# Kernel optimization log

Measured on AMD Instinct MI355X. Metric: run time of the kernel, lower is better.

The kernel has to match this reference:

```python
import jax, jax.numpy as jnp
import numpy as np

B, V, H_DIM, W_DIM = 4, 4, 256, 384
D_SH = 1  # sh_degree=0, pred_color=False -> (0+1)^2
SCALE_MIN, SCALE_MAX = 1e-05, 30.0
EPS = 1e-08


def _quat_to_mat(q):  # (...,4) wxyz unit quat -> (...,3,3)
    w, x, y, z = q[..., 0], q[..., 1], q[..., 2], q[..., 3]
    return jnp.stack([
        jnp.stack([1 - 2 * (y * y + z * z), 2 * (x * y - w * z), 2 * (x * z + w * y)], -1),
        jnp.stack([2 * (x * y + w * z), 1 - 2 * (x * x + z * z), 2 * (y * z - w * x)], -1),
        jnp.stack([2 * (x * z - w * y), 2 * (y * z + w * x), 1 - 2 * (x * x + y * y)], -1),
    ], -2)


def _mat_to_quat_wxyz(m):  # (...,3,3) rotation -> (...,4) wxyz
    m00, m01, m02 = m[..., 0, 0], m[..., 0, 1], m[..., 0, 2]
    m10, m11, m12 = m[..., 1, 0], m[..., 1, 1], m[..., 1, 2]
    m20, m21, m22 = m[..., 2, 0], m[..., 2, 1], m[..., 2, 2]
    q_abs = jnp.sqrt(jnp.maximum(0.0, jnp.stack([
        1.0 + m00 + m11 + m22, 1.0 + m00 - m11 - m22,
        1.0 - m00 + m11 - m22, 1.0 - m00 - m11 + m22], -1)))
    cand = jnp.stack([
        jnp.stack([q_abs[..., 0] ** 2, m21 - m12, m02 - m20, m10 - m01], -1),
        jnp.stack([m21 - m12, q_abs[..., 1] ** 2, m10 + m01, m02 + m20], -1),
        jnp.stack([m02 - m20, m10 + m01, q_abs[..., 2] ** 2, m12 + m21], -1),
        jnp.stack([m10 - m01, m20 + m02, m21 + m12, q_abs[..., 3] ** 2], -1),
    ], -2)
    cand = cand / (2.0 * jnp.maximum(q_abs[..., None], 0.1))
    idx = jnp.argmax(q_abs, axis=-1)
    q = jnp.take_along_axis(cand, idx[..., None, None], axis=-2)[..., 0, :]
    return q / jnp.linalg.norm(q, axis=-1, keepdims=True)


def _quat_mul_wxyz(a, b):
    aw, ax, ay, az = a[..., 0], a[..., 1], a[..., 2], a[..., 3]
    bw, bx, by, bz = b[..., 0], b[..., 1], b[..., 2], b[..., 3]
    return jnp.stack([
        aw * bw - ax * bx - ay * by - az * bz,
        aw * bx + ax * bw + ay * bz - az * by,
        aw * by - ax * bz + ay * bw + az * bx,
        aw * bz + ax * by - ay * bx + az * bw], -1)


def setup_inputs() -> dict:
    key = jax.random.key(0)
    k1, k2, k3, k4, k5, k6 = jax.random.split(key, 6)
    # valid world->cam extrinsics: rotation from random unit quats + translation
    q = jax.random.normal(k1, (B, V, 4), jnp.float32)
    q = q / jnp.linalg.norm(q, axis=-1, keepdims=True)
    R = _quat_to_mat(q)
    t = jax.random.normal(k2, (B, V, 3), jnp.float32)
    ext = jnp.zeros((B, V, 4, 4), jnp.float32)
    ext = ext.at[..., :3, :3].set(R).at[..., :3, 3].set(t).at[..., 3, 3].set(1.0)
    # pixel-unit intrinsics
    f = W_DIM * (0.8 + 0.4 * jax.random.uniform(k3, (B, V), jnp.float32))
    intr = jnp.zeros((B, V, 3, 3), jnp.float32)
    intr = (intr.at[..., 0, 0].set(f).at[..., 1, 1].set(f)
                .at[..., 0, 2].set(W_DIM / 2).at[..., 1, 2].set(H_DIM / 2)
                .at[..., 2, 2].set(1.0))
    depths = 0.5 + 9.5 * jax.random.uniform(k4, (B, V, H_DIM, W_DIM), jnp.float32)
    opac = jax.random.uniform(k5, (B, V, H_DIM, W_DIM), jnp.float32)
    raw = jax.random.normal(k6, (B, V, H_DIM, W_DIM, 12), jnp.float32)
    return {"extrinsics": ext, "intrinsics": intr, "depths": depths,
            "opacities": opac, "raw_gaussians": raw, "H": H_DIM, "W": W_DIM}


def reference(extrinsics, intrinsics, depths, opacities, raw_gaussians, H, W):
    raw = raw_gaussians
    b, v = raw.shape[:2]
    dtype = raw.dtype
    # cam2world = affine inverse of world2cam extrinsics
    Rw2c = extrinsics[..., :3, :3]
    t = extrinsics[..., :3, 3]
    Rc2w = jnp.swapaxes(Rw2c, -1, -2)                       # (b,v,3,3)
    origins = -jnp.einsum('bvij,bvj->bvi', Rc2w, t)          # (b,v,3) camera centers
    # normalized intrinsics (detached in the original)
    intr_n = jax.lax.stop_gradient(intrinsics) * jnp.array(
        [[1.0 / W], [1.0 / H], [1.0]], dtype=intrinsics.dtype)
    # pixel-center grid in normalized [0,1] coords, (x, y) order
    xs = (jnp.arange(W, dtype=dtype) + 0.5) / W
    ys = (jnp.arange(H, dtype=dtype) + 0.5) / H
    xy = jnp.stack(jnp.meshgrid(xs, ys, indexing='xy'), -1)  # (H,W,2)
    pixel_size = jnp.array([1.0 / W, 1.0 / H], dtype=dtype)
    xy = xy[None, None] + raw[..., :2] * pixel_size          # (b,v,H,W,2) with xy offset
    # unproject: K^-1 @ [x,y,1], normalize, rotate into world
    Kinv = jnp.linalg.inv(intr_n)                            # (b,v,3,3)
    homog = jnp.concatenate([xy, jnp.ones_like(xy[..., :1])], -1)
    d_cam = jnp.einsum('bvij,bvhwj->bvhwi', Kinv, homog)
    d_cam = d_cam / jnp.linalg.norm(d_cam, axis=-1, keepdims=True)
    d_world = jnp.einsum('bvij,bvhwj->bvhwi', Rc2w, d_cam)
    means = origins[:, :, None, None] + d_world * depths[..., None]
    means = means.reshape(b, -1, 3)
    # scales: sigmoid squash then metric scaling by depth * intrinsics multiplier
    scales = SCALE_MIN + (SCALE_MAX - SCALE_MIN) * jax.nn.sigmoid(raw[..., 2:5])
    k2 = intr_n[..., :2, :2]
    det = k2[..., 0, 0] * k2[..., 1, 1] - k2[..., 0, 1] * k2[..., 1, 0]
    inv2 = jnp.stack([
        jnp.stack([k2[..., 1, 1], -k2[..., 0, 1]], -1),
        jnp.stack([-k2[..., 1, 0], k2[..., 0, 0]], -1)], -2) / det[..., None, None]
    mult = 0.1 * jnp.einsum('bvij,j->bvi', inv2, pixel_size).sum(-1)  # (b,v)
    gs_scales = (scales * depths[..., None] * mult[:, :, None, None, None]).reshape(b, -1, 3)
    # rotations: normalize predicted cam quat (xyzw), compose with c2w rotation -> world wxyz
    rot = raw[..., 5:9]
    rot = rot / (jnp.linalg.norm(rot, axis=-1, keepdims=True) + EPS)
    cam_q_wxyz = jnp.concatenate([rot[..., 3:4], rot[..., :3]], -1)
    c2w_q = _mat_to_quat_wxyz(Rc2w)                          # (b,v,4)
    world_q = _quat_mul_wxyz(c2w_q[:, :, None, None, :], cam_q_wxyz)
    rotations = world_q.reshape(b, -1, 4)
    # spherical harmonics: degree 0 -> sh_mask is all ones, no SH rotation
    harmonics = raw[..., 9:12].reshape(b, -1, 3, D_SH)
    opac = opacities.reshape(b, -1)
    return means, gs_scales, rotations, harmonics, opac
```

## Files before the change

### kernel.cpp

```cpp
#include <hip/hip_runtime.h>
#include <math.h>

#define Bc 4
#define Vc 4
#define Hc 256
#define Wc 384
#define HWc (Hc*Wc)
#define TOTc (Bc*Vc*HWc)
#define SCALE_MIN_c 1e-05f
#define SCALE_MAX_c 30.0f
#define EPS_c 1e-08f

#define MEANS_OFF  ((size_t)0)
#define SCALES_OFF ((size_t)TOTc*3)
#define ROT_OFF    ((size_t)TOTc*6)
#define HARM_OFF   ((size_t)TOTc*10)
#define OPAC_OFF   ((size_t)TOTc*13)

__global__ __launch_bounds__(256) void ga_kernel(
    const float* __restrict__ ext,
    const float* __restrict__ intr,
    const float* __restrict__ depths,
    const float* __restrict__ opac,
    const float* __restrict__ raw,
    float* __restrict__ out)
{
    __shared__ float sR[9];
    __shared__ float sO[3];
    __shared__ float sK[9];
    __shared__ float sQ[4];
    __shared__ float sMult;

    const int tid = threadIdx.x;
    const int g   = blockIdx.x * 256 + tid;

    if (tid == 0) {
        const int view = blockIdx.x / (HWc / 256);
        const float* E = ext + view * 16;
        float R[9];
        #pragma unroll
        for (int i = 0; i < 3; i++)
            #pragma unroll
            for (int j = 0; j < 3; j++)
                R[i*3+j] = E[j*4+i];
        const float t0 = E[3], t1 = E[7], t2 = E[11];
        sO[0] = -(R[0]*t0 + R[1]*t1 + R[2]*t2);
        sO[1] = -(R[3]*t0 + R[4]*t1 + R[5]*t2);
        sO[2] = -(R[6]*t0 + R[7]*t1 + R[8]*t2);
        #pragma unroll
        for (int k = 0; k < 9; k++) sR[k] = R[k];

        const float* I = intr + view * 9;
        const float a00 = I[0]*(1.0f/Wc), a01 = I[1]*(1.0f/Wc), a02 = I[2]*(1.0f/Wc);
        const float a10 = I[3]*(1.0f/Hc), a11 = I[4]*(1.0f/Hc), a12 = I[5]*(1.0f/Hc);
        const float a20 = I[6],           a21 = I[7],           a22 = I[8];
        const float det = a00*(a11*a22 - a12*a21)
                        - a01*(a10*a22 - a12*a20)
                        + a02*(a10*a21 - a11*a20);
        const float id = 1.0f / det;
        sK[0] = (a11*a22 - a12*a21)*id;
        sK[1] = (a02*a21 - a01*a22)*id;
        sK[2] = (a01*a12 - a02*a11)*id;
        sK[3] = (a12*a20 - a10*a22)*id;
        sK[4] = (a00*a22 - a02*a20)*id;
        sK[5] = (a02*a10 - a00*a12)*id;
        sK[6] = (a10*a21 - a11*a20)*id;
        sK[7] = (a01*a20 - a00*a21)*id;
        sK[8] = (a00*a11 - a01*a10)*id;

        const float det2 = a00*a11 - a01*a10;
        const float psx = 1.0f/Wc, psy = 1.0f/Hc;
        sMult = 0.1f * ((a11*psx - a01*psy) + (-a10*psx + a00*psy)) / det2;

        const float m00 = R[0], m01 = R[1], m02 = R[2];
        const float m10 = R[3], m11 = R[4], m12 = R[5];
        const float m20 = R[6], m21 = R[7], m22 = R[8];
        float qa[4];
        qa[0] = sqrtf(fmaxf(0.0f, 1.0f + m00 + m11 + m22));
        qa[1] = sqrtf(fmaxf(0.0f, 1.0f + m00 - m11 - m22));
        qa[2] = sqrtf(fmaxf(0.0f, 1.0f - m00 + m11 - m22));
        qa[3] = sqrtf(fmaxf(0.0f, 1.0f - m00 - m11 + m22));
        float cand[4][4] = {
            { qa[0]*qa[0], m21 - m12,   m02 - m20,   m10 - m01 },
            { m21 - m12,   qa[1]*qa[1], m10 + m01,   m02 + m20 },
            { m02 - m20,   m10 + m01,   qa[2]*qa[2], m12 + m21 },
            { m10 - m01,   m20 + m02,   m21 + m12,   qa[3]*qa[3] } };
        int idx = 0;
        if (qa[1] > qa[idx]) idx = 1;
        if (qa[2] > qa[idx]) idx = 2;
        if (qa[3] > qa[idx]) idx = 3;
        const float dd = 1.0f / (2.0f * fmaxf(qa[idx], 0.1f));
        float q0 = cand[idx][0]*dd, q1 = cand[idx][1]*dd,
              q2 = cand[idx][2]*dd, q3 = cand[idx][3]*dd;
        const float qn = 1.0f / sqrtf(q0*q0 + q1*q1 + q2*q2 + q3*q3);
        sQ[0] = q0*qn; sQ[1] = q1*qn; sQ[2] = q2*qn; sQ[3] = q3*qn;
    }
    __syncthreads();

    const float4* rp = reinterpret_cast<const float4*>(raw + (size_t)g * 12);
    const float4 r0 = rp[0];
    const float4 r1 = rp[1];
    const float4 r2 = rp[2];

    const int pix = g % HWc;
    const int h = pix / Wc;
    const int w = pix % Wc;

    const float x = (w + 0.5f) * (1.0f/Wc) + r0.x * (1.0f/Wc);
    const float y = (h + 0.5f) * (1.0f/Hc) + r0.y * (1.0f/Hc);

    float dc0 = sK[0]*x + sK[1]*y + sK[2];
    float dc1 = sK[3]*x + sK[4]*y + sK[5];
    float dc2 = sK[6]*x + sK[7]*y + sK[8];
    const float inl = rsqrtf(dc0*dc0 + dc1*dc1 + dc2*dc2);
    dc0 *= inl; dc1 *= inl; dc2 *= inl;

    const float dw0 = sR[0]*dc0 + sR[1]*dc1 + sR[2]*dc2;
    const float dw1 = sR[3]*dc0 + sR[4]*dc1 + sR[5]*dc2;
    const float dw2 = sR[6]*dc0 + sR[7]*dc1 + sR[8]*dc2;

    const float dep = depths[g];

    out[MEANS_OFF + (size_t)g*3 + 0] = sO[0] + dw0 * dep;
    out[MEANS_OFF + (size_t)g*3 + 1] = sO[1] + dw1 * dep;
    out[MEANS_OFF + (size_t)g*3 + 2] = sO[2] + dw2 * dep;

    const float sm = dep * sMult;
    const float s0 = (SCALE_MIN_c + (SCALE_MAX_c - SCALE_MIN_c) / (1.0f + __expf(-r0.z))) * sm;
    const float s1 = (SCALE_MIN_c + (SCALE_MAX_c - SCALE_MIN_c) / (1.0f + __expf(-r0.w))) * sm;
    const float s2 = (SCALE_MIN_c + (SCALE_MAX_c - SCALE_MIN_c) / (1.0f + __expf(-r1.x))) * sm;
    out[SCALES_OFF + (size_t)g*3 + 0] = s0;
    out[SCALES_OFF + (size_t)g*3 + 1] = s1;
    out[SCALES_OFF + (size_t)g*3 + 2] = s2;

    const float rx = r1.y, ry = r1.z, rz = r1.w, rw = r2.x;
    const float rn = 1.0f / (sqrtf(rx*rx + ry*ry + rz*rz + rw*rw) + EPS_c);
    const float bw = rw*rn, bx = rx*rn, by = ry*rn, bz = rz*rn;
    const float aw = sQ[0], ax = sQ[1], ay = sQ[2], az = sQ[3];
    float4 wq;
    wq.x = aw*bw - ax*bx - ay*by - az*bz;
    wq.y = aw*bx + ax*bw + ay*bz - az*by;
    wq.z = aw*by - ax*bz + ay*bw + az*bx;
    wq.w = aw*bz + ax*by - ay*bx + az*bw;
    reinterpret_cast<float4*>(out + ROT_OFF)[g] = wq;

    out[HARM_OFF + (size_t)g*3 + 0] = r2.y;
    out[HARM_OFF + (size_t)g*3 + 1] = r2.z;
    out[HARM_OFF + (size_t)g*3 + 2] = r2.w;

    out[OPAC_OFF + g] = opac[g];
}

extern "C" void kernel_launch(void* const* d_in, const int* in_sizes, int n_in,
                              void* d_out, int out_size, void* d_ws, size_t ws_size,
                              hipStream_t stream) {
    const float* ext    = (const float*)d_in[0];
    const float* intr   = (const float*)d_in[1];
    const float* depths = (const float*)d_in[2];
    const float* opac   = (const float*)d_in[3];
    const float* raw    = (const float*)d_in[4];
    float* out = (float*)d_out;

    ga_kernel<<<TOTc / 256, 256, 0, stream>>>(ext, intr, depths, opac, raw, out);
}
```

Before: 170.4 us.

## Stage stride-3 outputs through shared memory for coalesced float4 stores

The means, scales and harmonics outputs, which were written as scalar stride-3 stores, are now gathered in a shared-memory tile and written back as contiguous float4 stores per block. The global loads of raw, depth and opacity are moved ahead of the thread-0 camera setup and the first barrier, so they can overlap with it. This adds 9 KB of LDS per block and a second barrier, which may lower occupancy.

```diff
diff --git a/kernel.cpp b/kernel.cpp
--- a/kernel.cpp
+++ b/kernel.cpp
@@ -30,9 +30,17 @@
     __shared__ float sK[9];
     __shared__ float sQ[4];
     __shared__ float sMult;
+    __shared__ float sOut[2304];
 
     const int tid = threadIdx.x;
     const int g   = blockIdx.x * 256 + tid;
+
+    const float4* rp = reinterpret_cast<const float4*>(raw + (size_t)g * 12);
+    const float4 r0 = rp[0];
+    const float4 r1 = rp[1];
+    const float4 r2 = rp[2];
+    const float dep = depths[g];
+    const float op  = opac[g];
 
     if (tid == 0) {
         const int view = blockIdx.x / (HWc / 256);
@@ -97,11 +105,6 @@
     }
     __syncthreads();
 
-    const float4* rp = reinterpret_cast<const float4*>(raw + (size_t)g * 12);
-    const float4 r0 = rp[0];
-    const float4 r1 = rp[1];
-    const float4 r2 = rp[2];
-
     const int pix = g % HWc;
     const int h = pix / Wc;
     const int w = pix % Wc;
@@ -119,19 +122,14 @@
     const float dw1 = sR[3]*dc0 + sR[4]*dc1 + sR[5]*dc2;
     const float dw2 = sR[6]*dc0 + sR[7]*dc1 + sR[8]*dc2;
 
-    const float dep = depths[g];
-
-    out[MEANS_OFF + (size_t)g*3 + 0] = sO[0] + dw0 * dep;
-    out[MEANS_OFF + (size_t)g*3 + 1] = sO[1] + dw1 * dep;
-    out[MEANS_OFF + (size_t)g*3 + 2] = sO[2] + dw2 * dep;
+    sOut[tid*3 + 0] = sO[0] + dw0 * dep;
+    sOut[tid*3 + 1] = sO[1] + dw1 * dep;
+    sOut[tid*3 + 2] = sO[2] + dw2 * dep;
 
     const float sm = dep * sMult;
-    const float s0 = (SCALE_MIN_c + (SCALE_MAX_c - SCALE_MIN_c) / (1.0f + __expf(-r0.z))) * sm;
-    const float s1 = (SCALE_MIN_c + (SCALE_MAX_c - SCALE_MIN_c) / (1.0f + __expf(-r0.w))) * sm;
-    const float s2 = (SCALE_MIN_c + (SCALE_MAX_c - SCALE_MIN_c) / (1.0f + __expf(-r1.x))) * sm;
-    out[SCALES_OFF + (size_t)g*3 + 0] = s0;
-    out[SCALES_OFF + (size_t)g*3 + 1] = s1;
-    out[SCALES_OFF + (size_t)g*3 + 2] = s2;
+    sOut[768 + tid*3 + 0] = (SCALE_MIN_c + (SCALE_MAX_c - SCALE_MIN_c) / (1.0f + __expf(-r0.z))) * sm;
+    sOut[768 + tid*3 + 1] = (SCALE_MIN_c + (SCALE_MAX_c - SCALE_MIN_c) / (1.0f + __expf(-r0.w))) * sm;
+    sOut[768 + tid*3 + 2] = (SCALE_MIN_c + (SCALE_MAX_c - SCALE_MIN_c) / (1.0f + __expf(-r1.x))) * sm;
 
     const float rx = r1.y, ry = r1.z, rz = r1.w, rw = r2.x;
     const float rn = 1.0f / (sqrtf(rx*rx + ry*ry + rz*rz + rw*rw) + EPS_c);
@@ -144,11 +142,23 @@
     wq.w = aw*bz + ax*by - ay*bx + az*bw;
     reinterpret_cast<float4*>(out + ROT_OFF)[g] = wq;
 
-    out[HARM_OFF + (size_t)g*3 + 0] = r2.y;
-    out[HARM_OFF + (size_t)g*3 + 1] = r2.z;
-    out[HARM_OFF + (size_t)g*3 + 2] = r2.w;
+    sOut[1536 + tid*3 + 0] = r2.y;
+    sOut[1536 + tid*3 + 1] = r2.z;
+    sOut[1536 + tid*3 + 2] = r2.w;
 
-    out[OPAC_OFF + g] = opac[g];
+    out[OPAC_OFF + g] = op;
+
+    __syncthreads();
+
+    const float4* sv = reinterpret_cast<const float4*>(sOut);
+    #pragma unroll
+    for (int i = tid; i < 576; i += 256) {
+        const int sec = i / 192;
+        const int j   = i - sec * 192;
+        const size_t base = (sec == 0 ? MEANS_OFF : (sec == 1 ? SCALES_OFF : HARM_OFF))
+                          + (size_t)blockIdx.x * 768;
+        reinterpret_cast<float4*>(out + base)[j] = sv[i];
+    }
 }
 
 extern "C" void kernel_launch(void* const* d_in, const int* in_sizes, int n_in,
```

Result: no change. 170.6 us (+0.1%).

## Process four pixels per thread with vectorized stores and per-thread view setup

Applied to the files above, without the earlier changes.

Each thread now handles four consecutive pixels, loading raw/depth/opacity as 16-byte vectors and packing means, scales, harmonics and opacities into float4 nontemporal stores instead of scalar 3-strided stores. The per-view camera setup is computed redundantly by every thread in registers, removing the shared memory and __syncthreads barrier. The grid shrinks by four, which raises register pressure and per-thread setup cost in exchange for wider, fully coalesced memory transactions.

```diff
diff --git a/kernel.cpp b/kernel.cpp
--- a/kernel.cpp
+++ b/kernel.cpp
@@ -1,5 +1,7 @@
 #include <hip/hip_runtime.h>
 #include <math.h>
+
+typedef float f4 __attribute__((ext_vector_type(4)));
 
 #define Bc 4
 #define Vc 4
@@ -17,6 +19,8 @@
 #define HARM_OFF   ((size_t)TOTc*10)
 #define OPAC_OFF   ((size_t)TOTc*13)
 
+#define BLOCKS_PER_VIEW (HWc/1024)
+
 __global__ __launch_bounds__(256) void ga_kernel(
     const float* __restrict__ ext,
     const float* __restrict__ intr,
@@ -25,130 +29,142 @@
     const float* __restrict__ raw,
     float* __restrict__ out)
 {
-    __shared__ float sR[9];
-    __shared__ float sO[3];
-    __shared__ float sK[9];
-    __shared__ float sQ[4];
-    __shared__ float sMult;
+    const int tid  = threadIdx.x;
+    const int bid  = blockIdx.x;
+    const int view = bid / BLOCKS_PER_VIEW;
+    const int pix0 = (bid - view * BLOCKS_PER_VIEW) * 1024 + tid * 4;
+    const size_t g0 = (size_t)view * HWc + (size_t)pix0;
 
-    const int tid = threadIdx.x;
-    const int g   = blockIdx.x * 256 + tid;
+    const f4* rp = reinterpret_cast<const f4*>(raw + g0 * 12);
+    f4 rw[12];
+    #pragma unroll
+    for (int i = 0; i < 12; i++) rw[i] = rp[i];
+    const f4 dep4 = *reinterpret_cast<const f4*>(depths + g0);
+    const f4 op4  = *reinterpret_cast<const f4*>(opac + g0);
 
-    if (tid == 0) {
-        const int view = blockIdx.x / (HWc / 256);
-        const float* E = ext + view * 16;
-        float R[9];
-        #pragma unroll
-        for (int i = 0; i < 3; i++)
-            #pragma unroll
-            for (int j = 0; j < 3; j++)
-                R[i*3+j] = E[j*4+i];
-        const float t0 = E[3], t1 = E[7], t2 = E[11];
-        sO[0] = -(R[0]*t0 + R[1]*t1 + R[2]*t2);
-        sO[1] = -(R[3]*t0 + R[4]*t1 + R[5]*t2);
-        sO[2] = -(R[6]*t0 + R[7]*t1 + R[8]*t2);
-        #pragma unroll
-        for (int k = 0; k < 9; k++) sR[k] = R[k];
+    const float* E = ext + view * 16;
+    const float R0 = E[0], R1 = E[4], R2 = E[8];
+    const float R3 = E[1], R4 = E[5], R5 = E[9];
+    const float R6 = E[2], R7 = E[6], R8 = E[10];
+    const float t0 = E[3], t1 = E[7], t2 = E[11];
+    const float O0 = -(R0*t0 + R1*t1 + R2*t2);
+    const float O1 = -(R3*t0 + R4*t1 + R5*t2);
+    const float O2 = -(R6*t0 + R7*t1 + R8*t2);
 
-        const float* I = intr + view * 9;
-        const float a00 = I[0]*(1.0f/Wc), a01 = I[1]*(1.0f/Wc), a02 = I[2]*(1.0f/Wc);
-        const float a10 = I[3]*(1.0f/Hc), a11 = I[4]*(1.0f/Hc), a12 = I[5]*(1.0f/Hc);
-        const float a20 = I[6],           a21 = I[7],           a22 = I[8];
-        const float det = a00*(a11*a22 - a12*a21)
-                        - a01*(a10*a22 - a12*a20)
-                        + a02*(a10*a21 - a11*a20);
-        const float id = 1.0f / det;
-        sK[0] = (a11*a22 - a12*a21)*id;
-        sK[1] = (a02*a21 - a01*a22)*id;
-        sK[2] = (a01*a12 - a02*a11)*id;
-        sK[3] = (a12*a20 - a10*a22)*id;
-        sK[4] = (a00*a22 - a02*a20)*id;
-        sK[5] = (a02*a10 - a00*a12)*id;
-        sK[6] = (a10*a21 - a11*a20)*id;
-        sK[7] = (a01*a20 - a00*a21)*id;
-        sK[8] = (a00*a11 - a01*a10)*id;
+    const float* I = intr + view * 9;
+    const float a00 = I[0]*(1.0f/Wc), a01 = I[1]*(1.0f/Wc), a02 = I[2]*(1.0f/Wc);
+    const float a10 = I[3]*(1.0f/Hc), a11 = I[4]*(1.0f/Hc), a12 = I[5]*(1.0f/Hc);
+    const float a20 = I[6],           a21 = I[7],           a22 = I[8];
+    const float det = a00*(a11*a22 - a12*a21)
+                    - a01*(a10*a22 - a12*a20)
+                    + a02*(a10*a21 - a11*a20);
+    const float id = 1.0f / det;
+    const float K0 = (a11*a22 - a12*a21)*id;
+    const float K1 = (a02*a21 - a01*a22)*id;
+    const float K2 = (a01*a12 - a02*a11)*id;
+    const float K3 = (a12*a20 - a10*a22)*id;
+    const float K4 = (a00*a22 - a02*a20)*id;
+    const float K5 = (a02*a10 - a00*a12)*id;
+    const float K6 = (a10*a21 - a11*a20)*id;
+    const float K7 = (a01*a20 - a00*a21)*id;
+    const float K8 = (a00*a11 - a01*a10)*id;
 
-        const float det2 = a00*a11 - a01*a10;
-        const float psx = 1.0f/Wc, psy = 1.0f/Hc;
-        sMult = 0.1f * ((a11*psx - a01*psy) + (-a10*psx + a00*psy)) / det2;
+    const float det2 = a00*a11 - a01*a10;
+    const float psx = 1.0f/Wc, psy = 1.0f/Hc;
+    const float mult = 0.1f * ((a11*psx - a01*psy) + (-a10*psx + a00*psy)) / det2;
 
-        const float m00 = R[0], m01 = R[1], m02 = R[2];
-        const float m10 = R[3], m11 = R[4], m12 = R[5];
-        const float m20 = R[6], m21 = R[7], m22 = R[8];
-        float qa[4];
-        qa[0] = sqrtf(fmaxf(0.0f, 1.0f + m00 + m11 + m22));
-        qa[1] = sqrtf(fmaxf(0.0f, 1.0f + m00 - m11 - m22));
-        qa[2] = sqrtf(fmaxf(0.0f, 1.0f - m00 + m11 - m22));
-        qa[3] = sqrtf(fmaxf(0.0f, 1.0f - m00 - m11 + m22));
-        float cand[4][4] = {
-            { qa[0]*qa[0], m21 - m12,   m02 - m20,   m10 - m01 },
-            { m21 - m12,   qa[1]*qa[1], m10 + m01,   m02 + m20 },
-            { m02 - m20,   m10 + m01,   qa[2]*qa[2], m12 + m21 },
-            { m10 - m01,   m20 + m02,   m21 + m12,   qa[3]*qa[3] } };
-        int idx = 0;
-        if (qa[1] > qa[idx]) idx = 1;
-        if (qa[2] > qa[idx]) idx = 2;
-        if (qa[3] > qa[idx]) idx = 3;
-        const float dd = 1.0f / (2.0f * fmaxf(qa[idx], 0.1f));
-        float q0 = cand[idx][0]*dd, q1 = cand[idx][1]*dd,
-              q2 = cand[idx][2]*dd, q3 = cand[idx][3]*dd;
-        const float qn = 1.0f / sqrtf(q0*q0 + q1*q1 + q2*q2 + q3*q3);
-        sQ[0] = q0*qn; sQ[1] = q1*qn; sQ[2] = q2*qn; sQ[3] = q3*qn;
+    const float m00 = R0, m01 = R1, m02 = R2;
+    const float m10 = R3, m11 = R4, m12 = R5;
+    const float m20 = R6, m21 = R7, m22 = R8;
+    const float qa0 = sqrtf(fmaxf(0.0f, 1.0f + m00 + m11 + m22));
+    const float qa1 = sqrtf(fmaxf(0.0f, 1.0f + m00 - m11 - m22));
+    const float qa2 = sqrtf(fmaxf(0.0f, 1.0f - m00 + m11 - m22));
+    const float qa3 = sqrtf(fmaxf(0.0f, 1.0f - m00 - m11 + m22));
+    int idx = 0; float best = qa0, qsel = qa0;
+    if (qa1 > best) { idx = 1; best = qa1; }
+    if (qa2 > best) { idx = 2; best = qa2; }
+    if (qa3 > best) { idx = 3; best = qa3; }
+    float c0, c1, c2, c3;
+    if (idx == 0)      { c0 = qa0*qa0;   c1 = m21 - m12; c2 = m02 - m20; c3 = m10 - m01; qsel = qa0; }
+    else if (idx == 1) { c0 = m21 - m12; c1 = qa1*qa1;   c2 = m10 + m01; c3 = m02 + m20; qsel = qa1; }
+    else if (idx == 2) { c0 = m02 - m20; c1 = m10 + m01; c2 = qa2*qa2;   c3 = m12 + m21; qsel = qa2; }
+    else               { c0 = m10 - m01; c1 = m20 + m02; c2 = m21 + m12; c3 = qa3*qa3;   qsel = qa3; }
+    const float dd = 1.0f / (2.0f * fmaxf(qsel, 0.1f));
+    float q0 = c0*dd, q1 = c1*dd, q2 = c2*dd, q3 = c3*dd;
+    const float qn = 1.0f / sqrtf(q0*q0 + q1*q1 + q2*q2 + q3*q3);
+    const float aw = q0*qn, ax = q1*qn, ay = q2*qn, az = q3*qn;
+
+    const int h  = pix0 / Wc;
+    const int w0 = pix0 - h * Wc;
+    const float ybase = (h + 0.5f) * (1.0f/Hc);
+    const float dv[4] = { dep4.x, dep4.y, dep4.z, dep4.w };
+
+    f4 M[3], S[3], Hm[3], Rt[4];
+
+    #pragma unroll
+    for (int p = 0; p < 4; p++) {
+        const f4 ra = rw[3*p + 0];
+        const f4 rb = rw[3*p + 1];
+        const f4 rc = rw[3*p + 2];
+        const float dep = dv[p];
+
+        const float x = (w0 + p + 0.5f) * (1.0f/Wc) + ra.x * (1.0f/Wc);
+        const float y = ybase + ra.y * (1.0f/Hc);
+
+        float dc0 = K0*x + K1*y + K2;
+        float dc1 = K3*x + K4*y + K5;
+        float dc2 = K6*x + K7*y + K8;
+        const float inl = rsqrtf(dc0*dc0 + dc1*dc1 + dc2*dc2);
+        dc0 *= inl; dc1 *= inl; dc2 *= inl;
+
+        const float dw0 = R0*dc0 + R1*dc1 + R2*dc2;
+        const float dw1 = R3*dc0 + R4*dc1 + R5*dc2;
+        const float dw2 = R6*dc0 + R7*dc1 + R8*dc2;
+
+        M[(3*p+0)>>2][(3*p+0)&3] = O0 + dw0 * dep;
+        M[(3*p+1)>>2][(3*p+1)&3] = O1 + dw1 * dep;
+        M[(3*p+2)>>2][(3*p+2)&3] = O2 + dw2 * dep;
+
+        const float sm = dep * mult;
+        S[(3*p+0)>>2][(3*p+0)&3] = (SCALE_MIN_c + (SCALE_MAX_c - SCALE_MIN_c) / (1.0f + __expf(-ra.z))) * sm;
+        S[(3*p+1)>>2][(3*p+1)&3] = (SCALE_MIN_c + (SCALE_MAX_c - SCALE_MIN_c) / (1.0f + __expf(-ra.w))) * sm;
+        S[(3*p+2)>>2][(3*p+2)&3] = (SCALE_MIN_c + (SCALE_MAX_c - SCALE_MIN_c) / (1.0f + __expf(-rb.x))) * sm;
+
+        const float rx = rb.y, ry = rb.z, rz = rb.w, rwv = rc.x;
+        const float rn = 1.0f / (sqrtf(rx*rx + ry*ry + rz*rz + rwv*rwv) + EPS_c);
+        const float bw = rwv*rn, bx = rx*rn, by = ry*rn, bz = rz*rn;
+        f4 wq;
+        wq.x = aw*bw - ax*bx - ay*by - az*bz;
+        wq.y = aw*bx + ax*bw + ay*bz - az*by;
+        wq.z = aw*by - ax*bz + ay*bw + az*bx;
+        wq.w = aw*bz + ax*by - ay*bx + az*bw;
+        Rt[p] = wq;
+
+        Hm[(3*p+0)>>2][(3*p+0)&3] = rc.y;
+        Hm[(3*p+1)>>2][(3*p+1)&3] = rc.z;
+        Hm[(3*p+2)>>2][(3*p+2)&3] = rc.w;
     }
-    __syncthreads();
 
-    const float4* rp = reinterpret_cast<const float4*>(raw + (size_t)g * 12);
-    const float4 r0 = rp[0];
-    const float4 r1 = rp[1];
-    const float4 r2 = rp[2];
+    f4* mo = reinterpret_cast<f4*>(out + MEANS_OFF  + g0 * 3);
+    f4* so = reinterpret_cast<f4*>(out + SCALES_OFF + g0 * 3);
+    f4* ro = reinterpret_cast<f4*>(out + ROT_OFF    + g0 * 4);
+    f4* ho = reinterpret_cast<f4*>(out + HARM_OFF   + g0 * 3);
+    f4* oo = reinterpret_cast<f4*>(out + OPAC_OFF   + g0);
 
-    const int pix = g % HWc;
-    const int h = pix / Wc;
-    const int w = pix % Wc;
-
-    const float x = (w + 0.5f) * (1.0f/Wc) + r0.x * (1.0f/Wc);
-    const float y = (h + 0.5f) * (1.0f/Hc) + r0.y * (1.0f/Hc);
-
-    float dc0 = sK[0]*x + sK[1]*y + sK[2];
-    float dc1 = sK[3]*x + sK[4]*y + sK[5];
-    float dc2 = sK[6]*x + sK[7]*y + sK[8];
-    const float inl = rsqrtf(dc0*dc0 + dc1*dc1 + dc2*dc2);
-    dc0 *= inl; dc1 *= inl; dc2 *= inl;
-
-    const float dw0 = sR[0]*dc0 + sR[1]*dc1 + sR[2]*dc2;
-    const float dw1 = sR[3]*dc0 + sR[4]*dc1 + sR[5]*dc2;
-    const float dw2 = sR[6]*dc0 + sR[7]*dc1 + sR[8]*dc2;
-
-    const float dep = depths[g];
-
-    out[MEANS_OFF + (size_t)g*3 + 0] = sO[0] + dw0 * dep;
-    out[MEANS_OFF + (size_t)g*3 + 1] = sO[1] + dw1 * dep;
-    out[MEANS_OFF + (size_t)g*3 + 2] = sO[2] + dw2 * dep;
-
-    const float sm = dep * sMult;
-    const float s0 = (SCALE_MIN_c + (SCALE_MAX_c - SCALE_MIN_c) / (1.0f + __expf(-r0.z))) * sm;
-    const float s1 = (SCALE_MIN_c + (SCALE_MAX_c - SCALE_MIN_c) / (1.0f + __expf(-r0.w))) * sm;
-    const float s2 = (SCALE_MIN_c + (SCALE_MAX_c - SCALE_MIN_c) / (1.0f + __expf(-r1.x))) * sm;
-    out[SCALES_OFF + (size_t)g*3 + 0] = s0;
-    out[SCALES_OFF + (size_t)g*3 + 1] = s1;
-    out[SCALES_OFF + (size_t)g*3 + 2] = s2;
-
-    const float rx = r1.y, ry = r1.z, rz = r1.w, rw = r2.x;
-    const float rn = 1.0f / (sqrtf(rx*rx + ry*ry + rz*rz + rw*rw) + EPS_c);
-    const float bw = rw*rn, bx = rx*rn, by = ry*rn, bz = rz*rn;
-    const float aw = sQ[0], ax = sQ[1], ay = sQ[2], az = sQ[3];
-    float4 wq;
-    wq.x = aw*bw - ax*bx - ay*by - az*bz;
-    wq.y = aw*bx + ax*bw + ay*bz - az*by;
-    wq.z = aw*by - ax*bz + ay*bw + az*bx;
-    wq.w = aw*bz + ax*by - ay*bx + az*bw;
-    reinterpret_cast<float4*>(out + ROT_OFF)[g] = wq;
-
-    out[HARM_OFF + (size_t)g*3 + 0] = r2.y;
-    out[HARM_OFF + (size_t)g*3 + 1] = r2.z;
-    out[HARM_OFF + (size_t)g*3 + 2] = r2.w;
-
-    out[OPAC_OFF + g] = opac[g];
+    __builtin_nontemporal_store(M[0], mo + 0);
+    __builtin_nontemporal_store(M[1], mo + 1);
+    __builtin_nontemporal_store(M[2], mo + 2);
+    __builtin_nontemporal_store(S[0], so + 0);
+    __builtin_nontemporal_store(S[1], so + 1);
+    __builtin_nontemporal_store(S[2], so + 2);
+    __builtin_nontemporal_store(Rt[0], ro + 0);
+    __builtin_nontemporal_store(Rt[1], ro + 1);
+    __builtin_nontemporal_store(Rt[2], ro + 2);
+    __builtin_nontemporal_store(Rt[3], ro + 3);
+    __builtin_nontemporal_store(Hm[0], ho + 0);
+    __builtin_nontemporal_store(Hm[1], ho + 1);
+    __builtin_nontemporal_store(Hm[2], ho + 2);
+    __builtin_nontemporal_store(op4, oo);
 }
 
 extern "C" void kernel_launch(void* const* d_in, const int* in_sizes, int n_in,
@@ -161,5 +177,5 @@
     const float* raw    = (const float*)d_in[4];
     float* out = (float*)d_out;
 
-    ga_kernel<<<TOTc / 256, 256, 0, stream>>>(ext, intr, depths, opac, raw, out);
+    ga_kernel<<<TOTc / 1024, 256, 0, stream>>>(ext, intr, depths, opac, raw, out);
 }
```

Measured after the change: 212.1 us. 1.25x slower.
